# Performance work log

Hardware: AMD Instinct MI355X
Metric: run time of the kernel (lower is better)

Reference implementation:

```python
import jax, jax.numpy as jnp
import numpy as np

N_HEAD = 16
D_K = 64
D_V = 64
D_MODEL = 1024
EPS = 1e-6
NEG = -1e9


def layer_norm(x, gamma, beta):
    mu = jnp.mean(x, axis=-1, keepdims=True)
    var = jnp.var(x, axis=-1, keepdims=True)
    return (x - mu) * jax.lax.rsqrt(var + EPS) * gamma + beta


def setup_inputs() -> dict:
    key = jax.random.key(0)
    ks = jax.random.split(key, 8)
    B, L = 2, 2048
    q = jax.random.normal(ks[0], (B, L, D_MODEL), dtype=jnp.float32)
    k = jax.random.normal(ks[1], (B, L, D_MODEL), dtype=jnp.float32)
    v = jax.random.normal(ks[2], (B, L, D_MODEL), dtype=jnp.float32)
    mask = jnp.ones((L, L), dtype=jnp.int32)
    s = 1.0 / np.sqrt(D_MODEL)
    w_q = jax.random.normal(ks[3], (N_HEAD * D_K, D_MODEL), dtype=jnp.float32) * s
    w_k = jax.random.normal(ks[4], (N_HEAD * D_K, D_MODEL), dtype=jnp.float32) * s
    w_v = jax.random.normal(ks[5], (N_HEAD * D_V, D_MODEL), dtype=jnp.float32) * s
    w_o = jax.random.normal(ks[6], (D_MODEL, N_HEAD * D_V), dtype=jnp.float32) * s
    ln_g = jnp.ones((D_MODEL,), dtype=jnp.float32)
    ln_b = jnp.zeros((D_MODEL,), dtype=jnp.float32)
    return {"q": q, "k": k, "v": v, "mask": mask,
            "w_q": w_q, "w_k": w_k, "w_v": w_v, "w_o": w_o,
            "ln_g": ln_g, "ln_b": ln_b}


def reference(q, k, v, mask, w_q, w_k, w_v, w_o, ln_g, ln_b):
    B, Lq, _ = q.shape
    Lk = k.shape[1]
    residual = q
    qn = layer_norm(q, ln_g, ln_b)
    # projections (nn.Linear: x @ W^T), reshape to [B, H, L, d]
    Q = (qn @ w_q.T).reshape(B, Lq, N_HEAD, D_K).transpose(0, 2, 1, 3)
    K = (k @ w_k.T).reshape(B, Lk, N_HEAD, D_K).transpose(0, 2, 1, 3)
    V = (v @ w_v.T).reshape(B, Lk, N_HEAD, D_V).transpose(0, 2, 1, 3)
    temp = jnp.asarray(D_K ** 0.5, dtype=Q.dtype)
    attn = jnp.einsum('bhqd,bhkd->bhqk', Q / temp, K)
    attn = jnp.where(mask[None, None] == 0, jnp.asarray(NEG, attn.dtype), attn)
    attn = jax.nn.softmax(attn, axis=-1)  # dropout is identity in eval
    out = jnp.einsum('bhqk,bhkd->bhqd', attn, V)
    out = out.transpose(0, 2, 1, 3).reshape(B, Lq, N_HEAD * D_V)
    out = out @ w_o.T
    return out + residual
```

## Files before the change

kernel.cpp:

```cpp
#include <hip/hip_runtime.h>
#include <stdint.h>

typedef __attribute__((ext_vector_type(8))) short bf16x8;
typedef __attribute__((ext_vector_type(4))) short s16x4;
typedef __attribute__((ext_vector_type(4))) float f32x4;
typedef __attribute__((ext_vector_type(16))) float f32x16;

__device__ __forceinline__ ushort f2bf(float f) {
  union { float f; uint32_t u; } c; c.f = f;
  uint32_t r = (c.u + 0x7fffu + ((c.u >> 16) & 1u)) >> 16;
  return (ushort)r;
}

__device__ __forceinline__ void gload16(const void* g, void* l) {
  __builtin_amdgcn_global_load_lds(
      (const __attribute__((address_space(1))) void*)g,
      (__attribute__((address_space(3))) void*)l, 16, 0, 0);
}

__device__ __forceinline__ unsigned lds_addr(const void* p) {
  return (unsigned)(uintptr_t)(__attribute__((address_space(3))) const char*)p;
}

__device__ __forceinline__ uint32_t cvtpk(float lo, float hi) {
  uint32_t d;
  asm("v_cvt_pk_bf16_f32 %0, %1, %2" : "=v"(d) : "v"(lo), "v"(hi));
  return d;
}

__global__ __launch_bounds__(256) void prep_kernel(
    const float* __restrict__ q, const float* __restrict__ k,
    const float* __restrict__ v, const float* __restrict__ w_q,
    const float* __restrict__ w_k, const float* __restrict__ w_v,
    const float* __restrict__ w_o, const float* __restrict__ ln_g,
    const float* __restrict__ ln_b,
    ushort* __restrict__ qn, ushort* __restrict__ kb, ushort* __restrict__ vb,
    ushort* __restrict__ wqb, ushort* __restrict__ wkb,
    ushort* __restrict__ wvb, ushort* __restrict__ wob) {
  const int bid = blockIdx.x;
  const int t = threadIdx.x;
  if (bid < 4096) {
    const int row = bid;
    const float4 val = ((const float4*)(q + (size_t)row * 1024))[t];
    float s  = val.x + val.y + val.z + val.w;
    float s2 = val.x*val.x + val.y*val.y + val.z*val.z + val.w*val.w;
    #pragma unroll
    for (int off = 1; off < 64; off <<= 1) {
      s  += __shfl_xor(s,  off);
      s2 += __shfl_xor(s2, off);
    }
    __shared__ float red[8];
    const int wave = t >> 6, lane = t & 63;
    if (lane == 0) { red[wave*2] = s; red[wave*2+1] = s2; }
    __syncthreads();
    s  = red[0] + red[2] + red[4] + red[6];
    s2 = red[1] + red[3] + red[5] + red[7];
    const float mu = s * (1.0f/1024.0f);
    const float var = s2 * (1.0f/1024.0f) - mu*mu;
    const float rs = rsqrtf(var + 1e-6f);
    const float4 gg = ((const float4*)ln_g)[t];
    const float4 bb = ((const float4*)ln_b)[t];
    ushort4 o;
    o.x = f2bf((val.x - mu) * rs * gg.x + bb.x);
    o.y = f2bf((val.y - mu) * rs * gg.y + bb.y);
    o.z = f2bf((val.z - mu) * rs * gg.z + bb.z);
    o.w = f2bf((val.w - mu) * rs * gg.w + bb.w);
    ((ushort4*)(qn + (size_t)row * 1024))[t] = o;
    return;
  }
  const float* in; ushort* out; int i;
  if (bid < 12288) {
    const int idx = bid - 4096;
    const bool isv = idx >= 4096;
    in  = isv ? v : k;
    out = isv ? vb : kb;
    i = (idx & 4095) * 256 + t;
  } else {
    const int idx = bid - 12288;
    const int w = idx >> 10;
    in  = w == 0 ? w_q : (w == 1 ? w_k : (w == 2 ? w_v : w_o));
    out = w == 0 ? wqb : (w == 1 ? wkb : (w == 2 ? wvb : wob));
    i = (idx & 1023) * 256 + t;
  }
  const float4 val = ((const float4*)in)[i];
  ushort4 o;
  o.x = f2bf(val.x); o.y = f2bf(val.y); o.z = f2bf(val.z); o.w = f2bf(val.w);
  ((ushort4*)out)[i] = o;
}

__global__ __launch_bounds__(256) void mask_flags(
    const int* __restrict__ mask, int* __restrict__ flags) {
  const int qt = blockIdx.y, kt = blockIdx.x;
  const int t = threadIdx.x;
  const int* p = mask + (size_t)(qt * 64 + (t >> 2)) * 2048 + kt * 64 + (t & 3) * 16;
  int ok = 1;
  #pragma unroll
  for (int i = 0; i < 4; i++) {
    const int4 m = ((const int4*)p)[i];
    ok &= (m.x != 0) & (m.y != 0) & (m.z != 0) & (m.w != 0);
  }
  __shared__ int sok;
  if (t == 0) sok = 1;
  __syncthreads();
  if (!ok) atomicAnd(&sok, 0);
  __syncthreads();
  if (t == 0) flags[qt * 32 + kt] = sok;
}

__global__ __launch_bounds__(256, 3) void gemm3(
    const ushort* __restrict__ A0, const ushort* __restrict__ W0, ushort* __restrict__ C0,
    const ushort* __restrict__ A1, const ushort* __restrict__ W1, ushort* __restrict__ C1,
    const ushort* __restrict__ A2, const ushort* __restrict__ W2, ushort* __restrict__ C2,
    float qscale) {
  __shared__ ushort As[3][4096];
  __shared__ ushort Bs[3][4096];
  const int t = threadIdx.x, lane = t & 63, wave = t >> 6;
  const int wr = wave >> 1, wc = wave & 1;
  const int lr = lane & 15, lg = lane >> 4;
  const int lin = blockIdx.x;
  const int swz = (lin & 7) * 96 + (lin >> 3);
  const int brow = ((swz >> 3) & 31) * 128, bcol = (swz & 7) * 128;
  const int z = swz >> 8;
  const ushort* A = z == 0 ? A0 : (z == 1 ? A1 : A2);
  const ushort* W = z == 0 ? W0 : (z == 1 ? W1 : W2);
  ushort*      C = z == 0 ? C0 : (z == 1 ? C1 : C2);
  const float sc = (z == 0) ? qscale : 1.0f;
  f32x4 acc[4][4] = {};
  const int r_ = t >> 2, cx = (t & 3) ^ ((r_ >> 1) & 3);
  const ushort* gA  = A + (size_t)(brow + r_) * 1024 + cx * 8;
  const ushort* gB  = W + (size_t)(bcol + r_) * 1024 + cx * 8;
  const ushort* gA2 = gA + 64 * 1024;
  const ushort* gB2 = gB + 64 * 1024;
  const int woff = wave * 1024;
  char* const la0 = (char*)As[0] + woff;
  char* const la1 = (char*)As[1] + woff;
  char* const la2 = (char*)As[2] + woff;
  char* const lb0 = (char*)Bs[0] + woff;
  char* const lb1 = (char*)Bs[1] + woff;
  char* const lb2 = (char*)Bs[2] + woff;
  const int xA = ((lr >> 1) & 3) * 8;

#define G_ISSUE_U(LA, LB, OFF) { \
    gload16(gA  + (OFF), (LA));        gload16(gA2 + (OFF), (LA) + 4096); \
    gload16(gB  + (OFF), (LB));        gload16(gB2 + (OFF), (LB) + 4096); }

#define G_COMPUTE_U(BI) { \
    const ushort* as_ = As[BI]; \
    const ushort* bs_ = Bs[BI]; \
    bf16x8 af[4], bfr[4]; \
    _Pragma("unroll") for (int i = 0; i < 4; i++) \
      af[i]  = *(const bf16x8*)&as_[(wr*64 + i*16 + lr) * 32 + ((lg*8) ^ xA)]; \
    _Pragma("unroll") for (int i = 0; i < 4; i++) \
      bfr[i] = *(const bf16x8*)&bs_[(wc*64 + i*16 + lr) * 32 + ((lg*8) ^ xA)]; \
    _Pragma("unroll") for (int mi = 0; mi < 4; mi++) \
      _Pragma("unroll") for (int ni = 0; ni < 4; ni++) \
        acc[mi][ni] = __builtin_amdgcn_mfma_f32_16x16x32_bf16(af[mi], bfr[ni], acc[mi][ni], 0, 0, 0); }

  G_ISSUE_U(la0, lb0, 0);
  G_ISSUE_U(la1, lb1, 32);
  for (int k = 0; k < 10; ++k) {
    asm volatile("s_waitcnt vmcnt(4)" ::: "memory");
    __builtin_amdgcn_s_barrier();
    G_ISSUE_U(la2, lb2, 64);
    G_COMPUTE_U(0);
    asm volatile("s_waitcnt vmcnt(4)" ::: "memory");
    __builtin_amdgcn_s_barrier();
    G_ISSUE_U(la0, lb0, 96);
    G_COMPUTE_U(1);
    asm volatile("s_waitcnt vmcnt(4)" ::: "memory");
    __builtin_amdgcn_s_barrier();
    G_ISSUE_U(la1, lb1, 128);
    G_COMPUTE_U(2);
    gA += 96; gA2 += 96; gB += 96; gB2 += 96;
  }
  asm volatile("s_waitcnt vmcnt(4)" ::: "memory");
  __builtin_amdgcn_s_barrier();
  G_COMPUTE_U(0);
  asm volatile("s_waitcnt vmcnt(0)" ::: "memory");
  __builtin_amdgcn_s_barrier();
  G_COMPUTE_U(1);
#undef G_ISSUE_U
#undef G_COMPUTE_U

  #pragma unroll
  for (int mi = 0; mi < 4; mi++) {
    #pragma unroll
    for (int ni = 0; ni < 4; ni++) {
      #pragma unroll
      for (int r = 0; r < 4; r++) {
        const size_t row = brow + wr*64 + mi*16 + lg*4 + r;
        const size_t col = bcol + wc*64 + ni*16 + lr;
        C[row * 1024 + col] = f2bf(acc[mi][ni][r] * sc);
      }
    }
  }
}

__global__ __launch_bounds__(256) void gemm_bm64(
    const ushort* __restrict__ A, const ushort* __restrict__ W,
    float* __restrict__ Cf, const float* __restrict__ resid) {
  __shared__ ushort As[4][2048];
  __shared__ ushort Bs[4][4096];
  const int t = threadIdx.x, lane = t & 63, wave = t >> 6;
  const int wr = wave >> 1, wc = wave & 1;
  const int lr = lane & 15, lg = lane >> 4;
  const int lin = blockIdx.x;
  const int swz = (lin & 7) * 64 + (lin >> 3);
  const int brow = (swz >> 3) * 64, bcol = (swz & 7) * 128;
  f32x4 acc[2][4] = {};
  const int r_ = t >> 2, cx = (t & 3) ^ ((r_ >> 1) & 3);
  const ushort* gA = A + (size_t)(brow + r_) * 1024 + cx * 8;
  const ushort* gB = W + (size_t)(bcol + r_) * 1024 + cx * 8;
  const int woff = wave * 1024;
  const int xA = ((lr >> 1) & 3) * 8;

#define G_ISSUE(S) { \
    char* la = (char*)As + ((S) & 3) * 4096 + woff; \
    char* lb = (char*)Bs + ((S) & 3) * 8192 + woff; \
    const ushort* ap_ = gA + (S) * 32; \
    const ushort* bp_ = gB + (S) * 32; \
    gload16(ap_, la); \
    gload16(bp_, lb); gload16(bp_ + 64 * 1024, lb + 4096); }

#define G_COMPUTE(S) { \
    const ushort* as_ = As[(S) & 3]; \
    const ushort* bs_ = Bs[(S) & 3]; \
    bf16x8 af[2], bfr[4]; \
    _Pragma("unroll") for (int i = 0; i < 2; i++) \
      af[i]  = *(const bf16x8*)&as_[(wr*32 + i*16 + lr) * 32 + ((lg*8) ^ xA)]; \
    _Pragma("unroll") for (int i = 0; i < 4; i++) \
      bfr[i] = *(const bf16x8*)&bs_[(wc*64 + i*16 + lr) * 32 + ((lg*8) ^ xA)]; \
    _Pragma("unroll") for (int mi = 0; mi < 2; mi++) \
      _Pragma("unroll") for (int ni = 0; ni < 4; ni++) \
        acc[mi][ni] = __builtin_amdgcn_mfma_f32_16x16x32_bf16(af[mi], bfr[ni], acc[mi][ni], 0, 0, 0); }

  G_ISSUE(0); G_ISSUE(1); G_ISSUE(2);
  for (int s = 0; s < 30; ++s) {
    asm volatile("s_waitcnt vmcnt(6)" ::: "memory");
    __builtin_amdgcn_s_barrier();
    if (s < 29) G_ISSUE(s + 3);
    G_COMPUTE(s);
  }
  asm volatile("s_waitcnt vmcnt(3)" ::: "memory");
  __builtin_amdgcn_s_barrier();
  G_COMPUTE(30);
  asm volatile("s_waitcnt vmcnt(0)" ::: "memory");
  __builtin_amdgcn_s_barrier();
  G_COMPUTE(31);
#undef G_ISSUE
#undef G_COMPUTE

  #pragma unroll
  for (int mi = 0; mi < 2; mi++) {
    #pragma unroll
    for (int ni = 0; ni < 4; ni++) {
      #pragma unroll
      for (int r = 0; r < 4; r++) {
        const size_t row = brow + wr*32 + mi*16 + lg*4 + r;
        const size_t col = bcol + wc*64 + ni*16 + lr;
        Cf[row * 1024 + col] = acc[mi][ni][r] + resid[row * 1024 + col];
      }
    }
  }
}

__global__ __launch_bounds__(256) void flash_attn(
    const ushort* __restrict__ Qp, const ushort* __restrict__ Kp,
    const ushort* __restrict__ Vp, const int* __restrict__ mask,
    const int* __restrict__ tflags, ushort* __restrict__ AO) {
  const int L = 2048;
  const int lin = blockIdx.x;
  const int swzb = (lin & 7) * 64 + (lin >> 3);
  const int qb = swzb & 15, h = (swzb >> 4) & 15, b = swzb >> 8;
  const int t = threadIdx.x, lane = t & 63, wave = t >> 6;
  const int l31 = lane & 31, hi = lane >> 5;
  __shared__ ushort Ks[2][8192];
  __shared__ ushort Vs[2][8192];
  const size_t base = (size_t)b * L * 1024 + h * 64;
  const int qw0 = qb * 128 + wave * 32;

  bf16x8 qf[4];
  #pragma unroll
  for (int kc = 0; kc < 4; kc++)
    qf[kc] = *(const bf16x8*)(Qp + base + (size_t)(qw0 + l31) * 1024 + kc*16 + hi*8);

  f32x16 accO0 = {0.f}, accO1 = {0.f}, accL = {0.f};
  const bf16x8 onef = {16256, 16256, 16256, 16256, 16256, 16256, 16256, 16256};

  const int r3 = (lane >> 3) & 7;
  const int c3 = (lane & 7) ^ r3;
  const ushort* gK = Kp + base + (size_t)(wave*8 + r3) * 1024 + c3 * 8;
  const int sv = t >> 3, hv = t & 7;
  const int vkv = (sv >> 2) * 4 + (hv >> 1);
  const int vd  = (sv & 3) * 16 + (hv & 1) * 8;
  const ushort* gV = Vp + base + (size_t)vkv * 1024 + vd;

  const unsigned vbase = lds_addr((const char*)Vs) + hi * 1024 +
                         ((lane >> 4) & 1) * 128 + (lane & 15) * 8;
  const int rx = (l31 & 7) << 4;

#define STAGE2(P, BUF) { \
    char* kb_ = (char*)Ks[BUF] + wave * 1024; \
    const ushort* gk_ = gK + (size_t)(2*(P)) * 65536; \
    gload16(gk_,             kb_);         gload16(gk_ + 32*1024, kb_ + 4096); \
    gload16(gk_ + 64*1024,   kb_ + 8192);  gload16(gk_ + 96*1024, kb_ + 12288); \
    char* vb_ = (char*)Vs[BUF] + wave * 1024; \
    const ushort* gv_ = gV + (size_t)(2*(P)) * 65536; \
    gload16(gv_,             vb_);         gload16(gv_ + 32*1024, vb_ + 4096); \
    gload16(gv_ + 64*1024,   vb_ + 8192);  gload16(gv_ + 96*1024, vb_ + 12288); }

#define TRREAD(VLO, VHI, VA) { \
    _Pragma("unroll") for (int dblk = 0; dblk < 2; dblk++) \
      _Pragma("unroll") for (int kc = 0; kc < 4; kc++) \
        asm volatile("ds_read_b64_tr_b16 %0, %2 offset:%3\n\t" \
                     "ds_read_b64_tr_b16 %1, %2 offset:%4" \
                     : "=v"(VLO[dblk][kc]), "=v"(VHI[dblk][kc]) \
                     : "v"(VA), "i"(kc*2048 + dblk*256), "i"(kc*2048 + dblk*256 + 512) \
                     : "memory"); }

#define QK(S0, S1, KSB) { \
    __builtin_amdgcn_s_setprio(1); \
    _Pragma("unroll") for (int kc = 0; kc < 4; kc++) { \
      const int xof = (kc*32 + hi*16) ^ rx; \
      const bf16x8 kf0 = *(const bf16x8*)((KSB) + l31 * 128 + xof); \
      const bf16x8 kf1 = *(const bf16x8*)((KSB) + (32 + l31) * 128 + xof); \
      S0 = __builtin_amdgcn_mfma_f32_32x32x16_bf16(kf0, qf[kc], S0, 0, 0, 0); \
      S1 = __builtin_amdgcn_mfma_f32_32x32x16_bf16(kf1, qf[kc], S1, 0, 0, 0); \
    } \
    __builtin_amdgcn_s_setprio(0); }

#define MASKT(S0, S1, KVT) \
    if (tflags[flagBase + (KVT)] == 0) { \
      const size_t mrow = (size_t)(qw0 + l31) * L + (KVT) * 64; \
      _Pragma("unroll") for (int r = 0; r < 16; ++r) { \
        const int kvr = (r & 3) + 8 * (r >> 2) + 4 * hi; \
        if (mask[mrow + kvr] == 0)      S0[r] = -1e9f; \
        if (mask[mrow + 32 + kvr] == 0) S1[r] = -1e9f; \
      } }

#define PACK(PA, S0, S1) { \
    union U8 { uint32_t u[4]; bf16x8 v; }; \
    _Pragma("unroll") for (int b2 = 0; b2 < 2; b2++) { \
      const f32x16& P = b2 ? S1 : S0; \
      uint32_t t0 = cvtpk(P[0], P[1]),  t1 = cvtpk(P[4], P[5]); \
      uint32_t u0 = cvtpk(P[2], P[3]),  u1 = cvtpk(P[6], P[7]); \
      asm("v_permlane32_swap_b32 %0, %1" : "+v"(t0), "+v"(t1)); \
      asm("v_permlane32_swap_b32 %0, %1" : "+v"(u0), "+v"(u1)); \
      U8 f0; f0.u[0] = t0; f0.u[1] = u0; f0.u[2] = t1; f0.u[3] = u1; \
      PA[2*b2] = f0.v; \
      uint32_t v0 = cvtpk(P[8], P[9]),   v1 = cvtpk(P[12], P[13]); \
      uint32_t w0 = cvtpk(P[10], P[11]), w1 = cvtpk(P[14], P[15]); \
      asm("v_permlane32_swap_b32 %0, %1" : "+v"(v0), "+v"(v1)); \
      asm("v_permlane32_swap_b32 %0, %1" : "+v"(w0), "+v"(w1)); \
      U8 f1; f1.u[0] = v0; f1.u[1] = w0; f1.u[2] = v1; f1.u[3] = w1; \
      PA[2*b2+1] = f1.v; \
    } }

#define PV(PA, VLO, VHI) { \
    __builtin_amdgcn_s_setprio(1); \
    _Pragma("unroll") for (int kc = 0; kc < 4; kc++) { \
      const bf16x8 bv0 = __builtin_shufflevector(VLO[0][kc], VHI[0][kc], \
                                                 0, 1, 2, 3, 4, 5, 6, 7); \
      accO0 = __builtin_amdgcn_mfma_f32_32x32x16_bf16(PA[kc], bv0, accO0, 0, 0, 0); \
      const bf16x8 bv1 = __builtin_shufflevector(VLO[1][kc], VHI[1][kc], \
                                                 0, 1, 2, 3, 4, 5, 6, 7); \
      accO1 = __builtin_amdgcn_mfma_f32_32x32x16_bf16(PA[kc], bv1, accO1, 0, 0, 0); \
      accL  = __builtin_amdgcn_mfma_f32_32x32x16_bf16(PA[kc], onef, accL, 0, 0, 0); \
    } \
    __builtin_amdgcn_s_setprio(0); }

  STAGE2(0, 0);
  const int flagBase = (qb * 2 + (wave >> 1)) * 32;

  for (int p = 0; p < 16; ++p) {
    asm volatile("s_waitcnt vmcnt(0)" ::: "memory");
    __builtin_amdgcn_s_barrier();
    if (p + 1 < 16) { STAGE2(p + 1, (p + 1) & 1); }

    const char* KsB0 = (const char*)Ks[p & 1];
    const char* KsB1 = KsB0 + 8192;
    const unsigned va0 = vbase + (p & 1) * 16384;

    f32x16 aS0 = {0.f}, aS1 = {0.f};
    QK(aS0, aS1, KsB0);

    s16x4 vlo0[2][4], vhi0[2][4];
    TRREAD(vlo0, vhi0, va0);

    f32x16 bS0 = {0.f}, bS1 = {0.f};
    QK(bS0, bS1, KsB1);

    MASKT(aS0, aS1, 2*p);
    #pragma unroll
    for (int r = 0; r < 16; ++r) {
      aS0[r] = __builtin_amdgcn_exp2f(aS0[r]);
      aS1[r] = __builtin_amdgcn_exp2f(aS1[r]);
    }
    bf16x8 pa0[4];
    PACK(pa0, aS0, aS1);

    asm volatile("s_waitcnt lgkmcnt(0)" ::: "memory");
    __builtin_amdgcn_sched_barrier(0);
    PV(pa0, vlo0, vhi0);

    s16x4 vlo1[2][4], vhi1[2][4];
    TRREAD(vlo1, vhi1, va0 + 8192);
    MASKT(bS0, bS1, 2*p + 1);
    #pragma unroll
    for (int r = 0; r < 16; ++r) {
      bS0[r] = __builtin_amdgcn_exp2f(bS0[r]);
      bS1[r] = __builtin_amdgcn_exp2f(bS1[r]);
    }
    bf16x8 pa1[4];
    PACK(pa1, bS0, bS1);

    asm volatile("s_waitcnt lgkmcnt(0)" ::: "memory");
    __builtin_amdgcn_sched_barrier(0);
    PV(pa1, vlo1, vhi1);
  }

  #pragma unroll
  for (int r = 0; r < 16; ++r) {
    const int qr = (r & 3) + 8 * (r >> 2) + 4 * hi;
    const float inv = 1.0f / accL[r];
    const size_t row = (size_t)b * L + qw0 + qr;
    AO[row * 1024 + h*64 +      l31] = f2bf(accO0[r] * inv);
    AO[row * 1024 + h*64 + 32 + l31] = f2bf(accO1[r] * inv);
  }
#undef STAGE2
#undef TRREAD
#undef QK
#undef MASKT
#undef PACK
#undef PV
}

extern "C" void kernel_launch(void* const* d_in, const int* in_sizes, int n_in,
                              void* d_out, int out_size, void* d_ws, size_t ws_size,
                              hipStream_t stream) {
  const float* q    = (const float*)d_in[0];
  const float* k    = (const float*)d_in[1];
  const float* v    = (const float*)d_in[2];
  const int*   mask = (const int*)d_in[3];
  const float* w_q  = (const float*)d_in[4];
  const float* w_k  = (const float*)d_in[5];
  const float* w_v  = (const float*)d_in[6];
  const float* w_o  = (const float*)d_in[7];
  const float* ln_g = (const float*)d_in[8];
  const float* ln_b = (const float*)d_in[9];
  float* out = (float*)d_out;

  char* ws = (char*)d_ws;
  const size_t MB = (size_t)1 << 20;
  ushort* qn  = (ushort*)(ws + 0*MB);
  ushort* kb  = (ushort*)(ws + 8*MB);
  ushort* vb  = (ushort*)(ws + 16*MB);
  ushort* wqb = (ushort*)(ws + 24*MB);
  ushort* wkb = (ushort*)(ws + 26*MB);
  ushort* wvb = (ushort*)(ws + 28*MB);
  ushort* wob = (ushort*)(ws + 30*MB);
  ushort* Qp  = (ushort*)(ws + 32*MB);
  ushort* Kp  = (ushort*)(ws + 40*MB);
  ushort* Vp  = (ushort*)(ws + 48*MB);
  ushort* AO  = (ushort*)(ws + 56*MB);
  int* tflags = (int*)(ws + 8*MB);

  const float QSCALE = 0.125f * 1.44269504089f;

  prep_kernel<<<16384, 256, 0, stream>>>(
      q, k, v, w_q, w_k, w_v, w_o, ln_g, ln_b,
      qn, kb, vb, wqb, wkb, wvb, wob);

  gemm3<<<768, 256, 0, stream>>>(
      qn, wqb, Qp, kb, wkb, Kp, vb, wvb, Vp, QSCALE);

  mask_flags<<<dim3(32, 32), 256, 0, stream>>>(mask, tflags);

  flash_attn<<<512, 256, 0, stream>>>(Qp, Kp, Vp, mask, tflags, AO);

  gemm_bm64<<<512, 256, 0, stream>>>(AO, wob, out, q);
}
```

Baseline: 132.7 us.

## Restructure flash attention to 8 waves of 16 query rows with 16x16 MFMA

The attention kernel now launches 512 threads per block (8 waves), each wave handling 16 query rows instead of 32. It switches from 32x32x16 to 16x16x32 MFMA tiles and rewrites the K/V staging, transposed V reads, mask handling and P packing (adding permlane16 swaps) to match. The aim is more waves per CU to hide latency with fewer registers per wave. In exchange, each K/V tile in LDS is reused by more waves, and the smaller MFMAs may lower matrix-core efficiency and add LDS read traffic per FLOP.

```diff
diff --git a/kernel.cpp b/kernel.cpp
--- a/kernel.cpp
+++ b/kernel.cpp
@@ -4,7 +4,6 @@
 typedef __attribute__((ext_vector_type(8))) short bf16x8;
 typedef __attribute__((ext_vector_type(4))) short s16x4;
 typedef __attribute__((ext_vector_type(4))) float f32x4;
-typedef __attribute__((ext_vector_type(16))) float f32x16;
 
 __device__ __forceinline__ ushort f2bf(float f) {
   union { float f; uint32_t u; } c; c.f = f;
@@ -264,7 +263,7 @@
   }
 }
 
-__global__ __launch_bounds__(256) void flash_attn(
+__global__ __launch_bounds__(512, 4) void flash_attn(
     const ushort* __restrict__ Qp, const ushort* __restrict__ Kp,
     const ushort* __restrict__ Vp, const int* __restrict__ mask,
     const int* __restrict__ tflags, ushort* __restrict__ AO) {
@@ -273,166 +272,152 @@
   const int swzb = (lin & 7) * 64 + (lin >> 3);
   const int qb = swzb & 15, h = (swzb >> 4) & 15, b = swzb >> 8;
   const int t = threadIdx.x, lane = t & 63, wave = t >> 6;
-  const int l31 = lane & 31, hi = lane >> 5;
+  const int l15 = lane & 15, hg = lane >> 4;
   __shared__ ushort Ks[2][8192];
   __shared__ ushort Vs[2][8192];
   const size_t base = (size_t)b * L * 1024 + h * 64;
-  const int qw0 = qb * 128 + wave * 32;
-
-  bf16x8 qf[4];
+  const int qw0 = qb * 128 + wave * 16;
+
+  bf16x8 qf[2];
   #pragma unroll
-  for (int kc = 0; kc < 4; kc++)
-    qf[kc] = *(const bf16x8*)(Qp + base + (size_t)(qw0 + l31) * 1024 + kc*16 + hi*8);
-
-  f32x16 accO0 = {0.f}, accO1 = {0.f}, accL = {0.f};
+  for (int kc = 0; kc < 2; kc++)
+    qf[kc] = *(const bf16x8*)(Qp + base + (size_t)(qw0 + l15) * 1024 + kc*32 + hg*8);
+
+  f32x4 accO[4] = {};
+  f32x4 accL = {};
   const bf16x8 onef = {16256, 16256, 16256, 16256, 16256, 16256, 16256, 16256};
 
-  const int r3 = (lane >> 3) & 7;
-  const int c3 = (lane & 7) ^ r3;
-  const ushort* gK = Kp + base + (size_t)(wave*8 + r3) * 1024 + c3 * 8;
-  const int sv = t >> 3, hv = t & 7;
-  const int vkv = (sv >> 2) * 4 + (hv >> 1);
-  const int vd  = (sv & 3) * 16 + (hv & 1) * 8;
+  const int r5 = t >> 3;
+  const ushort* gK = Kp + base + (size_t)r5 * 1024 + ((t & 7) ^ (r5 & 7)) * 8;
+  const int vkv = (t >> 5) * 4 + ((t & 7) >> 1);
+  const int vd  = ((t >> 3) & 3) * 16 + (t & 1) * 8;
   const ushort* gV = Vp + base + (size_t)vkv * 1024 + vd;
 
-  const unsigned vbase = lds_addr((const char*)Vs) + hi * 1024 +
-                         ((lane >> 4) & 1) * 128 + (lane & 15) * 8;
-  const int rx = (l31 & 7) << 4;
+  const unsigned vbase = lds_addr((const char*)Vs) + hg * 1024 + l15 * 8;
 
 #define STAGE2(P, BUF) { \
     char* kb_ = (char*)Ks[BUF] + wave * 1024; \
     const ushort* gk_ = gK + (size_t)(2*(P)) * 65536; \
-    gload16(gk_,             kb_);         gload16(gk_ + 32*1024, kb_ + 4096); \
-    gload16(gk_ + 64*1024,   kb_ + 8192);  gload16(gk_ + 96*1024, kb_ + 12288); \
+    gload16(gk_, kb_);           gload16(gk_ + 65536, kb_ + 8192); \
     char* vb_ = (char*)Vs[BUF] + wave * 1024; \
     const ushort* gv_ = gV + (size_t)(2*(P)) * 65536; \
-    gload16(gv_,             vb_);         gload16(gv_ + 32*1024, vb_ + 4096); \
-    gload16(gv_ + 64*1024,   vb_ + 8192);  gload16(gv_ + 96*1024, vb_ + 12288); }
-
-#define TRREAD(VLO, VHI, VA) { \
-    _Pragma("unroll") for (int dblk = 0; dblk < 2; dblk++) \
-      _Pragma("unroll") for (int kc = 0; kc < 4; kc++) \
-        asm volatile("ds_read_b64_tr_b16 %0, %2 offset:%3\n\t" \
-                     "ds_read_b64_tr_b16 %1, %2 offset:%4" \
-                     : "=v"(VLO[dblk][kc]), "=v"(VHI[dblk][kc]) \
-                     : "v"(VA), "i"(kc*2048 + dblk*256), "i"(kc*2048 + dblk*256 + 512) \
-                     : "memory"); }
-
-#define QK(S0, S1, KSB) { \
-    __builtin_amdgcn_s_setprio(1); \
-    _Pragma("unroll") for (int kc = 0; kc < 4; kc++) { \
-      const int xof = (kc*32 + hi*16) ^ rx; \
-      const bf16x8 kf0 = *(const bf16x8*)((KSB) + l31 * 128 + xof); \
-      const bf16x8 kf1 = *(const bf16x8*)((KSB) + (32 + l31) * 128 + xof); \
-      S0 = __builtin_amdgcn_mfma_f32_32x32x16_bf16(kf0, qf[kc], S0, 0, 0, 0); \
-      S1 = __builtin_amdgcn_mfma_f32_32x32x16_bf16(kf1, qf[kc], S1, 0, 0, 0); \
-    } \
-    __builtin_amdgcn_s_setprio(0); }
-
-#define MASKT(S0, S1, KVT) \
-    if (tflags[flagBase + (KVT)] == 0) { \
-      const size_t mrow = (size_t)(qw0 + l31) * L + (KVT) * 64; \
-      _Pragma("unroll") for (int r = 0; r < 16; ++r) { \
-        const int kvr = (r & 3) + 8 * (r >> 2) + 4 * hi; \
-        if (mask[mrow + kvr] == 0)      S0[r] = -1e9f; \
-        if (mask[mrow + 32 + kvr] == 0) S1[r] = -1e9f; \
-      } }
-
-#define PACK(PA, S0, S1) { \
-    union U8 { uint32_t u[4]; bf16x8 v; }; \
-    _Pragma("unroll") for (int b2 = 0; b2 < 2; b2++) { \
-      const f32x16& P = b2 ? S1 : S0; \
-      uint32_t t0 = cvtpk(P[0], P[1]),  t1 = cvtpk(P[4], P[5]); \
-      uint32_t u0 = cvtpk(P[2], P[3]),  u1 = cvtpk(P[6], P[7]); \
-      asm("v_permlane32_swap_b32 %0, %1" : "+v"(t0), "+v"(t1)); \
-      asm("v_permlane32_swap_b32 %0, %1" : "+v"(u0), "+v"(u1)); \
-      U8 f0; f0.u[0] = t0; f0.u[1] = u0; f0.u[2] = t1; f0.u[3] = u1; \
-      PA[2*b2] = f0.v; \
-      uint32_t v0 = cvtpk(P[8], P[9]),   v1 = cvtpk(P[12], P[13]); \
-      uint32_t w0 = cvtpk(P[10], P[11]), w1 = cvtpk(P[14], P[15]); \
-      asm("v_permlane32_swap_b32 %0, %1" : "+v"(v0), "+v"(v1)); \
-      asm("v_permlane32_swap_b32 %0, %1" : "+v"(w0), "+v"(w1)); \
-      U8 f1; f1.u[0] = v0; f1.u[1] = w0; f1.u[2] = v1; f1.u[3] = w1; \
-      PA[2*b2+1] = f1.v; \
-    } }
-
-#define PV(PA, VLO, VHI) { \
-    __builtin_amdgcn_s_setprio(1); \
-    _Pragma("unroll") for (int kc = 0; kc < 4; kc++) { \
-      const bf16x8 bv0 = __builtin_shufflevector(VLO[0][kc], VHI[0][kc], \
-                                                 0, 1, 2, 3, 4, 5, 6, 7); \
-      accO0 = __builtin_amdgcn_mfma_f32_32x32x16_bf16(PA[kc], bv0, accO0, 0, 0, 0); \
-      const bf16x8 bv1 = __builtin_shufflevector(VLO[1][kc], VHI[1][kc], \
-                                                 0, 1, 2, 3, 4, 5, 6, 7); \
-      accO1 = __builtin_amdgcn_mfma_f32_32x32x16_bf16(PA[kc], bv1, accO1, 0, 0, 0); \
-      accL  = __builtin_amdgcn_mfma_f32_32x32x16_bf16(PA[kc], onef, accL, 0, 0, 0); \
-    } \
-    __builtin_amdgcn_s_setprio(0); }
+    gload16(gv_, vb_);           gload16(gv_ + 65536, vb_ + 8192); }
+
+#define TRREAD(VLO, VHI, VA, C) { \
+    _Pragma("unroll") for (int dblk = 0; dblk < 4; dblk++) \
+      asm volatile("ds_read_b64_tr_b16 %0, %2 offset:%3\n\t" \
+                   "ds_read_b64_tr_b16 %1, %2 offset:%4" \
+                   : "=v"(VLO[dblk]), "=v"(VHI[dblk]) \
+                   : "v"(VA), "i"((C)*4096 + dblk*128), "i"((C)*4096 + dblk*128 + 512) \
+                   : "memory"); }
 
   STAGE2(0, 0);
-  const int flagBase = (qb * 2 + (wave >> 1)) * 32;
+  const int flagBase = (qb * 2 + (wave >> 2)) * 32;
 
   for (int p = 0; p < 16; ++p) {
     asm volatile("s_waitcnt vmcnt(0)" ::: "memory");
     __builtin_amdgcn_s_barrier();
     if (p + 1 < 16) { STAGE2(p + 1, (p + 1) & 1); }
 
-    const char* KsB0 = (const char*)Ks[p & 1];
-    const char* KsB1 = KsB0 + 8192;
-    const unsigned va0 = vbase + (p & 1) * 16384;
-
-    f32x16 aS0 = {0.f}, aS1 = {0.f};
-    QK(aS0, aS1, KsB0);
-
-    s16x4 vlo0[2][4], vhi0[2][4];
-    TRREAD(vlo0, vhi0, va0);
-
-    f32x16 bS0 = {0.f}, bS1 = {0.f};
-    QK(bS0, bS1, KsB1);
-
-    MASKT(aS0, aS1, 2*p);
     #pragma unroll
-    for (int r = 0; r < 16; ++r) {
-      aS0[r] = __builtin_amdgcn_exp2f(aS0[r]);
-      aS1[r] = __builtin_amdgcn_exp2f(aS1[r]);
+    for (int half = 0; half < 2; ++half) {
+      const int kvt = 2*p + half;
+      const char* KsB = (const char*)Ks[p & 1] + half * 8192;
+      const unsigned va = vbase + (p & 1) * 16384 + half * 8192;
+
+      f32x4 s0 = {0.f}, s1 = {0.f}, s2 = {0.f}, s3 = {0.f};
+      const int rx16 = (l15 & 7) << 4;
+      __builtin_amdgcn_s_setprio(1);
+      #pragma unroll
+      for (int kc = 0; kc < 2; kc++) {
+        const int cb = (kc*64 + hg*16) ^ rx16;
+        const bf16x8 k0 = *(const bf16x8*)(KsB + (     l15) * 128 + cb);
+        const bf16x8 k1 = *(const bf16x8*)(KsB + (16 + l15) * 128 + cb);
+        const bf16x8 k2 = *(const bf16x8*)(KsB + (32 + l15) * 128 + cb);
+        const bf16x8 k3 = *(const bf16x8*)(KsB + (48 + l15) * 128 + cb);
+        s0 = __builtin_amdgcn_mfma_f32_16x16x32_bf16(k0, qf[kc], s0, 0, 0, 0);
+        s1 = __builtin_amdgcn_mfma_f32_16x16x32_bf16(k1, qf[kc], s1, 0, 0, 0);
+        s2 = __builtin_amdgcn_mfma_f32_16x16x32_bf16(k2, qf[kc], s2, 0, 0, 0);
+        s3 = __builtin_amdgcn_mfma_f32_16x16x32_bf16(k3, qf[kc], s3, 0, 0, 0);
+      }
+      __builtin_amdgcn_s_setprio(0);
+
+      s16x4 vlo[4], vhi[4];
+      TRREAD(vlo, vhi, va, 0);
+
+      if (tflags[flagBase + kvt] == 0) {
+        const size_t mrow = (size_t)(qw0 + l15) * L + kvt * 64;
+        #pragma unroll
+        for (int r = 0; r < 4; ++r) {
+          const int kvr = hg*4 + r;
+          if (mask[mrow + kvr] == 0)      s0[r] = -1e9f;
+          if (mask[mrow + 16 + kvr] == 0) s1[r] = -1e9f;
+          if (mask[mrow + 32 + kvr] == 0) s2[r] = -1e9f;
+          if (mask[mrow + 48 + kvr] == 0) s3[r] = -1e9f;
+        }
+      }
+
+      #pragma unroll
+      for (int r = 0; r < 4; ++r) {
+        s0[r] = __builtin_amdgcn_exp2f(s0[r]);
+        s1[r] = __builtin_amdgcn_exp2f(s1[r]);
+        s2[r] = __builtin_amdgcn_exp2f(s2[r]);
+        s3[r] = __builtin_amdgcn_exp2f(s3[r]);
+      }
+
+      union U8 { uint32_t u[4]; bf16x8 v; };
+      bf16x8 pa[2];
+      #pragma unroll
+      for (int c = 0; c < 2; ++c) {
+        const f32x4& ta = c ? s2 : s0;
+        const f32x4& tb = c ? s3 : s1;
+        uint32_t A = cvtpk(ta[0], ta[1]), B = cvtpk(ta[2], ta[3]);
+        uint32_t C = cvtpk(tb[0], tb[1]), D = cvtpk(tb[2], tb[3]);
+        asm("v_permlane32_swap_b32 %0, %1" : "+v"(A), "+v"(C));
+        asm("v_permlane16_swap_b32 %0, %1" : "+v"(A), "+v"(C));
+        asm("v_permlane32_swap_b32 %0, %1" : "+v"(B), "+v"(D));
+        asm("v_permlane16_swap_b32 %0, %1" : "+v"(B), "+v"(D));
+        U8 f; f.u[0] = A; f.u[1] = B; f.u[2] = C; f.u[3] = D;
+        pa[c] = f.v;
+      }
+
+      asm volatile("s_waitcnt lgkmcnt(0)" ::: "memory");
+      __builtin_amdgcn_sched_barrier(0);
+      __builtin_amdgcn_s_setprio(1);
+      #pragma unroll
+      for (int dblk = 0; dblk < 4; dblk++) {
+        const bf16x8 bv = __builtin_shufflevector(vlo[dblk], vhi[dblk],
+                                                  0, 1, 2, 3, 4, 5, 6, 7);
+        accO[dblk] = __builtin_amdgcn_mfma_f32_16x16x32_bf16(pa[0], bv, accO[dblk], 0, 0, 0);
+      }
+      accL = __builtin_amdgcn_mfma_f32_16x16x32_bf16(pa[0], onef, accL, 0, 0, 0);
+      __builtin_amdgcn_s_setprio(0);
+
+      TRREAD(vlo, vhi, va, 1);
+      asm volatile("s_waitcnt lgkmcnt(0)" ::: "memory");
+      __builtin_amdgcn_sched_barrier(0);
+      __builtin_amdgcn_s_setprio(1);
+      #pragma unroll
+      for (int dblk = 0; dblk < 4; dblk++) {
+        const bf16x8 bv = __builtin_shufflevector(vlo[dblk], vhi[dblk],
+                                                  0, 1, 2, 3, 4, 5, 6, 7);
+        accO[dblk] = __builtin_amdgcn_mfma_f32_16x16x32_bf16(pa[1], bv, accO[dblk], 0, 0, 0);
+      }
+      accL = __builtin_amdgcn_mfma_f32_16x16x32_bf16(pa[1], onef, accL, 0, 0, 0);
+      __builtin_amdgcn_s_setprio(0);
     }
-    bf16x8 pa0[4];
-    PACK(pa0, aS0, aS1);
-
-    asm volatile("s_waitcnt lgkmcnt(0)" ::: "memory");
-    __builtin_amdgcn_sched_barrier(0);
-    PV(pa0, vlo0, vhi0);
-
-    s16x4 vlo1[2][4], vhi1[2][4];
-    TRREAD(vlo1, vhi1, va0 + 8192);
-    MASKT(bS0, bS1, 2*p + 1);
+  }
+
+  #pragma unroll
+  for (int r = 0; r < 4; ++r) {
+    const float inv = 1.0f / accL[r];
+    const size_t row = (size_t)b * L + qw0 + hg*4 + r;
     #pragma unroll
-    for (int r = 0; r < 16; ++r) {
-      bS0[r] = __builtin_amdgcn_exp2f(bS0[r]);
-      bS1[r] = __builtin_amdgcn_exp2f(bS1[r]);
-    }
-    bf16x8 pa1[4];
-    PACK(pa1, bS0, bS1);
-
-    asm volatile("s_waitcnt lgkmcnt(0)" ::: "memory");
-    __builtin_amdgcn_sched_barrier(0);
-    PV(pa1, vlo1, vhi1);
-  }
-
-  #pragma unroll
-  for (int r = 0; r < 16; ++r) {
-    const int qr = (r & 3) + 8 * (r >> 2) + 4 * hi;
-    const float inv = 1.0f / accL[r];
-    const size_t row = (size_t)b * L + qw0 + qr;
-    AO[row * 1024 + h*64 +      l31] = f2bf(accO0[r] * inv);
-    AO[row * 1024 + h*64 + 32 + l31] = f2bf(accO1[r] * inv);
+    for (int dblk = 0; dblk < 4; dblk++)
+      AO[row * 1024 + h*64 + dblk*16 + l15] = f2bf(accO[dblk][r] * inv);
   }
 #undef STAGE2
 #undef TRREAD
-#undef QK
-#undef MASKT
-#undef PACK
-#undef PV
 }
 
 extern "C" void kernel_launch(void* const* d_in, const int* in_sizes, int n_in,
@@ -476,7 +461,7 @@
 
   mask_flags<<<dim3(32, 32), 256, 0, stream>>>(mask, tflags);
 
-  flash_attn<<<512, 256, 0, stream>>>(Qp, Kp, Vp, mask, tflags, AO);
+  flash_attn<<<512, 512, 0, stream>>>(Qp, Kp, Vp, mask, tflags, AO);
 
   gemm_bm64<<<512, 256, 0, stream>>>(AO, wob, out, q);
 }
```

Result: faster. 124.9 us (-5.9%).
